# Kernel tuning notes

Hardware: AMD Instinct MI355X
Metric: run time of the kernel (lower is better)

## Reference

```python
import jax, jax.numpy as jnp
import numpy as np

HIDDEN = 128
N_HID = 7            # hidden_layers - 1 internal GELU blocks
N_TERMS = 2          # number of separable terms per side
N_IN = 1             # vars per term
B = 16384
STEP_SIZE = 0.1
NUM_STEPS = 1

# Forest-Ruth 4th-order symplectic coefficients
_K = 2.0 ** (1.0 / 3.0)
_C = (1.0 / (2.0 * (2.0 - _K)), (1.0 - _K) / (2.0 * (2.0 - _K)),
      (1.0 - _K) / (2.0 * (2.0 - _K)), 1.0 / (2.0 * (2.0 - _K)))
_D = (1.0 / (2.0 - _K), -_K / (2.0 - _K), 1.0 / (2.0 - _K), 0.0)


def _mlp(W0, b0, Wh, bh, Wo, bo, x):
    # x: [B, n_in] -> [B, 1]; torch GELU default is exact (erf)
    h = jax.nn.gelu(x @ W0 + b0, approximate=False)
    for i in range(N_HID):
        h = jax.nn.gelu(h @ Wh[i] + bh[i], approximate=False)
    return h @ Wo + bo


def _side_scalar(W0, b0, Wh, bh, Wo, bo, idx, x):
    # gather per-term feature subsets, run all term-MLPs batched via vmap,
    # sum over terms and batch (GradientWrapper takes grad of the summed scalar)
    xs = jnp.moveaxis(x[:, idx], 1, 0)            # [n_terms, B, n_in]
    outs = jax.vmap(_mlp)(W0, b0, Wh, bh, Wo, bo, xs)  # [n_terms, B, 1]
    return outs.sum()


def setup_inputs() -> dict:
    key = jax.random.key(0)
    ks = jax.random.split(key, 3)
    s = 0.05

    def pset(k):
        kk = jax.random.split(k, 6)
        return (
            jax.random.normal(kk[0], (N_TERMS, N_IN, HIDDEN), jnp.float32) * s,
            jax.random.normal(kk[1], (N_TERMS, HIDDEN), jnp.float32) * s,
            jax.random.normal(kk[2], (N_TERMS, N_HID, HIDDEN, HIDDEN), jnp.float32) * s,
            jax.random.normal(kk[3], (N_TERMS, N_HID, HIDDEN), jnp.float32) * s,
            jax.random.normal(kk[4], (N_TERMS, HIDDEN, 1), jnp.float32) * s,
            jax.random.normal(kk[5], (N_TERMS, 1), jnp.float32) * s,
        )

    lW0, lb0, lWh, lbh, lWo, lbo = pset(ks[0])
    rW0, rb0, rWh, rbh, rWo, rbo = pset(ks[1])
    X = jax.random.normal(ks[2], (B, 4), jnp.float32)
    left_idx = jnp.arange(N_TERMS, dtype=jnp.int32).reshape(N_TERMS, N_IN)
    right_idx = jnp.arange(N_TERMS, dtype=jnp.int32).reshape(N_TERMS, N_IN)
    return dict(X=X, lW0=lW0, lb0=lb0, lWh=lWh, lbh=lbh, lWo=lWo, lbo=lbo,
                rW0=rW0, rb0=rb0, rWh=rWh, rbh=rbh, rWo=rWo, rbo=rbo,
                left_idx=left_idx, right_idx=right_idx)


def reference(X, lW0, lb0, lWh, lbh, lWo, lbo,
              rW0, rb0, rWh, rbh, rWo, rbo, left_idx, right_idx):
    # H(q, p) = V(q) + T(p); left side = V(q), right side = T(p)
    dVdq = jax.grad(lambda q: _side_scalar(lW0, lb0, lWh, lbh, lWo, lbo, left_idx, q))
    dTdp = jax.grad(lambda p: _side_scalar(rW0, rb0, rWh, rbh, rWo, rbo, right_idx, p))
    dt = jnp.float32(STEP_SIZE)
    nq = X.shape[1] // 2
    q = X[:, :nq]
    p = X[:, nq:]
    for _ in range(NUM_STEPS):
        for c, d in zip(_C, _D):
            q = q + jnp.float32(c) * dt * dTdp(p)   # dq/dt =  dH/dp
            p = p - jnp.float32(d) * dt * dVdq(q)   # dp/dt = -dH/dq
    return jnp.concatenate((q, p), axis=1)
```

## Files before the change

kernel.cpp:

```cpp
#include <hip/hip_runtime.h>

#define NLAYER 7
#define IMGB 16384
#define WSCALE 16.0f

typedef __attribute__((ext_vector_type(2))) float float2v;
typedef __attribute__((ext_vector_type(4))) float float4v;
typedef __attribute__((ext_vector_type(4))) unsigned int uint4v;
typedef __attribute__((ext_vector_type(4))) int int4v;
typedef __attribute__((ext_vector_type(8))) int int8v;
typedef unsigned long long u64;

__device__ __forceinline__ float2v pk_fma(float2v a, float2v b, float2v c){
  return __builtin_elementwise_fma(a, b, c);
}
__device__ __forceinline__ float2v lo2(float4v v){ return (float2v){v[0], v[1]}; }
__device__ __forceinline__ float2v hi2(float4v v){ return (float2v){v[2], v[3]}; }

__device__ __forceinline__ unsigned pk4fp8(float v0, float v1, float v2, float v3){
  int w = __builtin_amdgcn_cvt_pk_fp8_f32(v0, v1, 0, false);
  w = __builtin_amdgcn_cvt_pk_fp8_f32(v2, v3, w, true);
  return (unsigned)w;
}
__device__ __forceinline__ float4v mfma128(int8v a, int8v b){
  return __builtin_amdgcn_mfma_scale_f32_16x16x128_f8f6f4(
      a, b, (float4v){0.f,0.f,0.f,0.f}, 0, 0, 0, 0x7F7F7F7F, 0, 0x7F7F7F7F);
}
__device__ __forceinline__ void act2(float2v z, float2v& P16, float2v& gp16){
  const float2v c1v  = {6.3830764862829235f, 6.3830764862829235f};
  const float2v c3v  = {-1.0638460810704874f, -1.0638460810704874f};
  const float2v c33v = {-3.1915382432114624f, -3.1915382432114624f};
  const float2v v8   = {8.f, 8.f};
  float2v z2 = z * z;
  float2v u  = pk_fma(z2, c3v, c1v);
  P16 = pk_fma(z, u, v8);
  float2v Pd = pk_fma(z2, c33v, c1v);
  gp16 = pk_fma(z, Pd, P16);
}

__device__ __forceinline__ void gl2lds16(const unsigned char* g, unsigned char* l){
  __builtin_amdgcn_global_load_lds((const __attribute__((address_space(1))) unsigned int*)g,
                                   (__attribute__((address_space(3))) unsigned int*)l,
                                   16, 0, 0);
}

__device__ __forceinline__ int8v ld_op16(const unsigned char* lp, const unsigned char* hp){
  int4v lo = *(const int4v*)lp;
  int4v hi = *(const int4v*)hp;
  return __builtin_shufflevector(lo, hi, 0, 1, 2, 3, 4, 5, 6, 7);
}

__global__ __launch_bounds__(256)
void prep_weights(const float* __restrict__ lWh,
                  const float* __restrict__ rWh,
                  unsigned char* __restrict__ wbf)
{
  __shared__ __align__(16) unsigned char T[IMGB];
  const int b = blockIdx.x;
  const int net = b / NLAYER, L = b % NLAYER;
  const int side = net >> 1, term = net & 1;
  const float* src = (side ? rWh : lWh) + (size_t)((term*NLAYER + L)*128)*128;
  const int t = threadIdx.x;
  {
    const int k = t >> 1, n0 = (t & 1)*64;
    const float* row = src + k*128 + n0;
    #pragma unroll
    for (int c4 = 0; c4 < 4; ++c4){
      float4v f0 = *(const float4v*)(row + c4*16);
      float4v f1 = *(const float4v*)(row + c4*16 + 4);
      float4v f2 = *(const float4v*)(row + c4*16 + 8);
      float4v f3 = *(const float4v*)(row + c4*16 + 12);
      uint4v wv = { pk4fp8(f0[0]*WSCALE, f0[1]*WSCALE, f0[2]*WSCALE, f0[3]*WSCALE),
                    pk4fp8(f1[0]*WSCALE, f1[1]*WSCALE, f1[2]*WSCALE, f1[3]*WSCALE),
                    pk4fp8(f2[0]*WSCALE, f2[1]*WSCALE, f2[2]*WSCALE, f2[3]*WSCALE),
                    pk4fp8(f3[0]*WSCALE, f3[1]*WSCALE, f3[2]*WSCALE, f3[3]*WSCALE) };
      *(uint4v*)&T[k*128 + n0 + c4*16] = wv;
    }
  }
  __syncthreads();
  {
    const int n = t >> 1, c0 = (t & 1)*8;
    const int sw7 = n & 7;
    unsigned char* dst = wbf + ((size_t)b << 14) + n*128;
    #pragma unroll
    for (int c = 0; c < 8; ++c){
      const int c64 = c0 + c;
      const int kc = c64*8;
      u64 v = 0;
      #pragma unroll
      for (int j = 0; j < 8; ++j)
        v |= (u64)T[(kc + j)*128 + n] << (8*j);
      *(u64*)(dst + (((c64 >> 1) ^ sw7)*16) + (c64 & 1)*8) = v;
    }
  }
}

__global__ __launch_bounds__(256)
__attribute__((amdgpu_waves_per_eu(2, 2)))
void sympl_main(const float* __restrict__ X,
                const float* __restrict__ lW0, const float* __restrict__ lb0,
                const float* __restrict__ lbh, const float* __restrict__ lWo,
                const float* __restrict__ rW0, const float* __restrict__ rb0,
                const float* __restrict__ rbh, const float* __restrict__ rWo,
                const int* __restrict__ lidx, const int* __restrict__ ridx,
                const unsigned char* __restrict__ wbf,
                float* __restrict__ out)
{
  __shared__ __align__(16) unsigned char sWb[2*IMGB];
  __shared__ __align__(16) unsigned char sH[4*4096];

  const int tid  = threadIdx.x;
  const int lane = tid & 63;
  const int w    = tid >> 6;
  const int m0   = lane & 15;
  const int q    = lane >> 4;
  const int q4   = q * 4;
  const int m06  = m0 & 6;
  const int m07  = m0 & 7;
  const int col  = blockIdx.y;
  const int e    = blockIdx.x*64 + w*16 + m0;

  const int lt = (lidx[0] == col) ? 0 : 1;
  const int rt = (ridx[0] == col) ? 0 : 1;

  float qv = X[e*4 + col];
  float pv = X[e*4 + 2 + col];

  const float dt = 0.1f;
  const float C0 = 0.6756035959798289f, C1 = -0.17560359597982883f;
  const float D0 = 1.3512071919596578f, D1 = -1.7024143839193153f;
  const float is = 1.0f / 262144.0f;
  const float coefs[7] = { C0*dt*is, -D0*dt*is, C1*dt*is, -D1*dt*is,
                           C1*dt*is, -D0*dt*is, C0*dt*is };

  const float2v inv256v = {1.f/256.f, 1.f/256.f};
  const float2v inv64v  = {1.f/64.f, 1.f/64.f};

  const int lo16 = (m0 & 1) * 16;
  const int opo  = ((2*q) ^ m06) * 16;
  const unsigned char* pAlo = sWb + m0*128 + opo + lo16;
  const unsigned char* pAhi = sWb + m0*128 + opo + 16 - lo16;
  unsigned char* pHw = sH + w*4096 + m0*128;
  const unsigned char* pBlo = pHw + opo + lo16;
  const unsigned char* pBhi = pHw + opo + 16 - lo16;

  {
    const unsigned char* src = wbf + (size_t)(2 + rt)*NLAYER*IMGB;
    #pragma unroll
    for (int it = 0; it < 4; ++it){
      int o = (it*256 + tid) * 16;
      gl2lds16(src + o, sWb + o);
    }
  }
  __syncthreads();

  for (int ev = 0; ev < 7; ++ev){
    const bool isT = !(ev & 1);
    const int  evp = ev & 1;
    const int  term = isT ? rt : lt;
    const float* W0p = (isT ? rW0 : lW0) + term*128;
    const float* b0p = (isT ? rb0 : lb0) + term*128;
    const float* bhp = (isT ? rbh : lbh) + term*NLAYER*128;
    const float* Wop = (isT ? rWo : lWo) + term*128;
    const unsigned char* wimg = wbf + (size_t)(((isT ? 2 : 0) + term)*NLAYER)*IMGB;
    const int tnx = (ev & 1) ? rt : lt;
    const unsigned char* wimg_nx = wbf + (size_t)((((ev & 1) ? 2 : 0) + tnx)*NLAYER)*IMGB;

    int8v b0, b1;
    {
      const float x = isT ? pv : qv;
      const float2v xv = {x, x};
      const float* Wq = W0p + q*32;
      const float* Bq = b0p + q*32;
      unsigned hwv[8], dwv[8];
      #pragma unroll
      for (int j = 0; j < 8; ++j){
        float4v wv4 = *(const float4v*)(Wq + j*4);
        float4v bb4 = *(const float4v*)(Bq + j*4);
        float2v zlo = pk_fma(xv, lo2(wv4), lo2(bb4));
        float2v zhi = pk_fma(xv, hi2(wv4), hi2(bb4));
        float2v Pl, gl, Ph, gh;
        act2(zlo, Pl, gl);
        act2(zhi, Ph, gh);
        float2v hl = zlo * Pl, hh = zhi * Ph;
        float2v dl = gl * lo2(wv4), dh = gh * hi2(wv4);
        hwv[j] = pk4fp8(hl[0], hl[1], hh[0], hh[1]);
        dwv[j] = pk4fp8(dl[0], dl[1], dh[0], dh[1]);
      }
      b0 = (int8v){(int)hwv[0],(int)hwv[1],(int)hwv[2],(int)hwv[3],
                   (int)hwv[4],(int)hwv[5],(int)hwv[6],(int)hwv[7]};
      b1 = (int8v){(int)dwv[0],(int)dwv[1],(int)dwv[2],(int)dwv[3],
                   (int)dwv[4],(int)dwv[5],(int)dwv[6],(int)dwv[7]};
    }

    float2v sv = {0.f, 0.f};

    #pragma unroll
    for (int L = 0; L < NLAYER; ++L){
      const int par  = (L & 1) ? (evp ^ 1) : evp;
      const int bufo = par ? IMGB : 0;
      const bool last = (L == NLAYER-1);

      const float* bias = bhp + L*128 + q4;
      float4v bvv[8];
      #pragma unroll
      for (int I = 0; I < 8; ++I) bvv[I] = *(const float4v*)(bias + I*16);
      float4v wov[8];
      if (last){
        #pragma unroll
        for (int I = 0; I < 8; ++I) wov[I] = *(const float4v*)(Wop + I*16 + q4);
      }

      if (!(ev == 6 && L == 6)){
        const unsigned char* nsrc = (L < 6) ? (wimg + (size_t)(L+1)*IMGB) : wimg_nx;
        unsigned char* dW = sWb + (bufo ^ IMGB);
        #pragma unroll
        for (int it = 0; it < 4; ++it){
          int o = (it*256 + tid) * 16;
          gl2lds16(nsrc + o, dW + o);
        }
      }

      const unsigned char* pAl = pAlo + bufo;
      const unsigned char* pAh = pAhi + bufo;
      #pragma unroll
      for (int I = 0; I < 8; ++I){
        int8v a = ld_op16(pAl + I*2048, pAh + I*2048);
        float4v aH = mfma128(a, b0);
        float4v aD = mfma128(a, b1);
        float2v za = pk_fma(lo2(aH), inv256v, lo2(bvv[I]));
        float2v zb = pk_fma(hi2(aH), inv256v, hi2(bvv[I]));
        float2v ta = lo2(aD) * inv64v;
        float2v tb = hi2(aD) * inv64v;
        float2v Pa, ga, Pb, gb;
        act2(za, Pa, ga);
        act2(zb, Pb, gb);
        float2v da = ga * ta, db = gb * tb;
        if (!last){
          float2v ha = za * Pa, hb = zb * Pb;
          const int eo = (I ^ m07)*16 + q4;
          *(unsigned*)(pHw + eo)        = pk4fp8(ha[0], ha[1], hb[0], hb[1]);
          *(unsigned*)(pHw + 2048 + eo) = pk4fp8(da[0], da[1], db[0], db[1]);
        } else {
          sv = pk_fma(da, lo2(wov[I]), sv);
          sv = pk_fma(db, hi2(wov[I]), sv);
        }
      }

      if (!last){
        b0 = ld_op16(pBlo, pBhi);
        b1 = ld_op16(pBlo + 2048, pBhi + 2048);
      }

      asm volatile("s_waitcnt vmcnt(0) lgkmcnt(0)" ::: "memory");
      __builtin_amdgcn_s_barrier();
      asm volatile("" ::: "memory");
    }

    {
      float s = sv[0] + sv[1];
      s += __shfl_xor(s, 16);
      s += __shfl_xor(s, 32);
      if (isT) qv += coefs[ev] * s;
      else     pv += coefs[ev] * s;
    }
  }

  if (q == 0){
    out[e*4 + col]     = qv;
    out[e*4 + 2 + col] = pv;
  }
}

extern "C" void kernel_launch(void* const* d_in, const int* in_sizes, int n_in,
                              void* d_out, int out_size, void* d_ws, size_t ws_size,
                              hipStream_t stream)
{
  const float* X   = (const float*)d_in[0];
  const float* lW0 = (const float*)d_in[1];
  const float* lb0 = (const float*)d_in[2];
  const float* lWh = (const float*)d_in[3];
  const float* lbh = (const float*)d_in[4];
  const float* lWo = (const float*)d_in[5];
  const float* rW0 = (const float*)d_in[7];
  const float* rb0 = (const float*)d_in[8];
  const float* rWh = (const float*)d_in[9];
  const float* rbh = (const float*)d_in[10];
  const float* rWo = (const float*)d_in[11];
  const int*   li  = (const int*)d_in[13];
  const int*   ri  = (const int*)d_in[14];
  unsigned char* wbf = (unsigned char*)d_ws;
  float* out = (float*)d_out;
  const int B = in_sizes[0] / 4;

  hipLaunchKernelGGL(prep_weights, dim3(4*NLAYER), dim3(256), 0, stream,
                     lWh, rWh, wbf);
  hipLaunchKernelGGL(sympl_main, dim3(B/64, 2), dim3(256), 0, stream,
                     X, lW0, lb0, lbh, lWo, rW0, rb0, rbh, rWo, li, ri, wbf, out);
}
```

Before: 192.8 us.

## Split hidden-unit output rows across two wave groups with 512-thread blocks

The block grows from 256 to 512 threads, and each group of four waves now computes half of the 128 output neurons for the same 64 samples, so per-wave MFMA and epilogue work is halved. Activations and their derivatives are exchanged through a double-buffered shared H buffer that all waves read back at the start of each layer. The final dot product with the output weights is reduced across the two halves through a small shared array. The intent is more waves per CU to hide latency. The cost is more LDS (sH grows to 32KB) and cross-wave data exchange every layer.

```diff
diff --git a/kernel.cpp b/kernel.cpp
--- a/kernel.cpp
+++ b/kernel.cpp
@@ -45,8 +45,8 @@
 }
 
 __device__ __forceinline__ int8v ld_op16(const unsigned char* lp, const unsigned char* hp){
-  int4v lo = *(const int4v*)lp;
-  int4v hi = *(const int4v*)hp;
+  int4v lo = *(const int4v*)(lp);
+  int4v hi = *(const int4v*)(hp);
   return __builtin_shufflevector(lo, hi, 0, 1, 2, 3, 4, 5, 6, 7);
 }
 
@@ -95,8 +95,8 @@
   }
 }
 
-__global__ __launch_bounds__(256)
-__attribute__((amdgpu_waves_per_eu(2, 2)))
+__global__ __launch_bounds__(512)
+__attribute__((amdgpu_waves_per_eu(4, 4)))
 void sympl_main(const float* __restrict__ X,
                 const float* __restrict__ lW0, const float* __restrict__ lb0,
                 const float* __restrict__ lbh, const float* __restrict__ lWo,
@@ -107,7 +107,8 @@
                 float* __restrict__ out)
 {
   __shared__ __align__(16) unsigned char sWb[2*IMGB];
-  __shared__ __align__(16) unsigned char sH[4*4096];
+  __shared__ __align__(16) unsigned char sH[2*16384];
+  __shared__ float sRed[2][64];
 
   const int tid  = threadIdx.x;
   const int lane = tid & 63;
@@ -115,10 +116,13 @@
   const int m0   = lane & 15;
   const int q    = lane >> 4;
   const int q4   = q * 4;
+  const int g2   = w & 3;
+  const int ih   = w >> 2;
   const int m06  = m0 & 6;
   const int m07  = m0 & 7;
   const int col  = blockIdx.y;
-  const int e    = blockIdx.x*64 + w*16 + m0;
+  const int le   = g2*16 + m0;
+  const int e    = blockIdx.x*64 + le;
 
   const int lt = (lidx[0] == col) ? 0 : 1;
   const int rt = (ridx[0] == col) ? 0 : 1;
@@ -138,17 +142,21 @@
 
   const int lo16 = (m0 & 1) * 16;
   const int opo  = ((2*q) ^ m06) * 16;
-  const unsigned char* pAlo = sWb + m0*128 + opo + lo16;
-  const unsigned char* pAhi = sWb + m0*128 + opo + 16 - lo16;
-  unsigned char* pHw = sH + w*4096 + m0*128;
-  const unsigned char* pBlo = pHw + opo + lo16;
-  const unsigned char* pBhi = pHw + opo + 16 - lo16;
+  const unsigned char* pBlo = sH + le*128 + opo + lo16;
+  const unsigned char* pBhi = sH + le*128 + opo + 16 - lo16;
+  const unsigned char* pAlo = sWb + (ih*64 + m0)*128 + opo + lo16;
+  const unsigned char* pAhi = sWb + (ih*64 + m0)*128 + opo + 16 - lo16;
+  unsigned char* pHe = sH + le*128;
+  unsigned char* pE0 = pHe + ((ih*4 + 0) ^ m07)*16 + q4;
+  unsigned char* pE1 = pHe + ((ih*4 + 1) ^ m07)*16 + q4;
+  unsigned char* pE2 = pHe + ((ih*4 + 2) ^ m07)*16 + q4;
+  unsigned char* pE3 = pHe + ((ih*4 + 3) ^ m07)*16 + q4;
 
   {
     const unsigned char* src = wbf + (size_t)(2 + rt)*NLAYER*IMGB;
     #pragma unroll
-    for (int it = 0; it < 4; ++it){
-      int o = (it*256 + tid) * 16;
+    for (int it = 0; it < 2; ++it){
+      int o = (it*512 + tid) * 16;
       gl2lds16(src + o, sWb + o);
     }
   }
@@ -197,59 +205,80 @@
 
     #pragma unroll
     for (int L = 0; L < NLAYER; ++L){
-      const int par  = (L & 1) ? (evp ^ 1) : evp;
+      const int rdo = (L & 1) * 16384;
+      const int wro = rdo ^ 16384;
+      const int par = (L & 1) ? (evp ^ 1) : evp;
       const int bufo = par ? IMGB : 0;
       const bool last = (L == NLAYER-1);
 
-      const float* bias = bhp + L*128 + q4;
-      float4v bvv[8];
-      #pragma unroll
-      for (int I = 0; I < 8; ++I) bvv[I] = *(const float4v*)(bias + I*16);
-      float4v wov[8];
+      const float* bias = bhp + L*128 + ih*64 + q4;
+      float4v bv0 = *(const float4v*)(bias);
+      float4v bv1 = *(const float4v*)(bias + 16);
+      float4v bv2 = *(const float4v*)(bias + 32);
+      float4v bv3 = *(const float4v*)(bias + 48);
+      float4v wo0, wo1, wo2, wo3;
       if (last){
-        #pragma unroll
-        for (int I = 0; I < 8; ++I) wov[I] = *(const float4v*)(Wop + I*16 + q4);
+        const float* wop = Wop + ih*64 + q4;
+        wo0 = *(const float4v*)(wop);
+        wo1 = *(const float4v*)(wop + 16);
+        wo2 = *(const float4v*)(wop + 32);
+        wo3 = *(const float4v*)(wop + 48);
       }
 
       if (!(ev == 6 && L == 6)){
         const unsigned char* nsrc = (L < 6) ? (wimg + (size_t)(L+1)*IMGB) : wimg_nx;
         unsigned char* dW = sWb + (bufo ^ IMGB);
         #pragma unroll
-        for (int it = 0; it < 4; ++it){
-          int o = (it*256 + tid) * 16;
+        for (int it = 0; it < 2; ++it){
+          int o = (it*512 + tid) * 16;
           gl2lds16(nsrc + o, dW + o);
         }
       }
 
+      if (L > 0){
+        b0 = ld_op16(pBlo + rdo, pBhi + rdo);
+        b1 = ld_op16(pBlo + rdo + 8192, pBhi + rdo + 8192);
+      }
+
       const unsigned char* pAl = pAlo + bufo;
       const unsigned char* pAh = pAhi + bufo;
+      float4v acc[4][2];
       #pragma unroll
-      for (int I = 0; I < 8; ++I){
-        int8v a = ld_op16(pAl + I*2048, pAh + I*2048);
-        float4v aH = mfma128(a, b0);
-        float4v aD = mfma128(a, b1);
-        float2v za = pk_fma(lo2(aH), inv256v, lo2(bvv[I]));
-        float2v zb = pk_fma(hi2(aH), inv256v, hi2(bvv[I]));
-        float2v ta = lo2(aD) * inv64v;
-        float2v tb = hi2(aD) * inv64v;
-        float2v Pa, ga, Pb, gb;
-        act2(za, Pa, ga);
-        act2(zb, Pb, gb);
-        float2v da = ga * ta, db = gb * tb;
-        if (!last){
-          float2v ha = za * Pa, hb = zb * Pb;
-          const int eo = (I ^ m07)*16 + q4;
-          *(unsigned*)(pHw + eo)        = pk4fp8(ha[0], ha[1], hb[0], hb[1]);
-          *(unsigned*)(pHw + 2048 + eo) = pk4fp8(da[0], da[1], db[0], db[1]);
-        } else {
-          sv = pk_fma(da, lo2(wov[I]), sv);
-          sv = pk_fma(db, hi2(wov[I]), sv);
-        }
-      }
-
-      if (!last){
-        b0 = ld_op16(pBlo, pBhi);
-        b1 = ld_op16(pBlo + 2048, pBhi + 2048);
+      for (int i = 0; i < 4; ++i){
+        int8v a = ld_op16(pAl + i*2048, pAh + i*2048);
+        acc[i][0] = mfma128(a, b0);
+        acc[i][1] = mfma128(a, b1);
+      }
+
+      #define EPI(i, bvv, wvv, pe) { \
+        float2v za = pk_fma(lo2(acc[i][0]), inv256v, lo2(bvv)); \
+        float2v zb = pk_fma(hi2(acc[i][0]), inv256v, hi2(bvv)); \
+        float2v ta = lo2(acc[i][1]) * inv64v; \
+        float2v tb = hi2(acc[i][1]) * inv64v; \
+        float2v Pa, ga, Pb, gb; \
+        act2(za, Pa, ga); \
+        act2(zb, Pb, gb); \
+        float2v da = ga * ta, db = gb * tb; \
+        if (!last){ \
+          float2v ha = za * Pa, hb = zb * Pb; \
+          *(unsigned*)(pe + wro)        = pk4fp8(ha[0], ha[1], hb[0], hb[1]); \
+          *(unsigned*)(pe + wro + 8192) = pk4fp8(da[0], da[1], db[0], db[1]); \
+        } else { \
+          sv = pk_fma(da, lo2(wvv), sv); \
+          sv = pk_fma(db, hi2(wvv), sv); \
+        } \
+      }
+      EPI(0, bv0, wo0, pE0)
+      EPI(1, bv1, wo1, pE1)
+      EPI(2, bv2, wo2, pE2)
+      EPI(3, bv3, wo3, pE3)
+      #undef EPI
+
+      if (last){
+        float sh = sv[0] + sv[1];
+        sh += __shfl_xor(sh, 16);
+        sh += __shfl_xor(sh, 32);
+        if (q == 0) sRed[ih][le] = sh;
       }
 
       asm volatile("s_waitcnt vmcnt(0) lgkmcnt(0)" ::: "memory");
@@ -258,15 +287,13 @@
     }
 
     {
-      float s = sv[0] + sv[1];
-      s += __shfl_xor(s, 16);
-      s += __shfl_xor(s, 32);
+      float s = sRed[0][le] + sRed[1][le];
       if (isT) qv += coefs[ev] * s;
       else     pv += coefs[ev] * s;
     }
   }
 
-  if (q == 0){
+  if (q == 0 && ih == 0){
     out[e*4 + col]     = qv;
     out[e*4 + 2 + col] = pv;
   }
@@ -295,6 +322,6 @@
 
   hipLaunchKernelGGL(prep_weights, dim3(4*NLAYER), dim3(256), 0, stream,
                      lWh, rWh, wbf);
-  hipLaunchKernelGGL(sympl_main, dim3(B/64, 2), dim3(256), 0, stream,
+  hipLaunchKernelGGL(sympl_main, dim3(B/64, 2), dim3(512), 0, stream,
                      X, lW0, lb0, lbh, lWo, rW0, rb0, rbh, rWo, li, ri, wbf, out);
 }
```

After: 186.4 us. 1.03x faster.
